# Optimization experiments

Hardware: AMD Instinct MI355X
Metric: run time of the kernel (lower is better)

## Reference

```python
import jax, jax.numpy as jnp
import numpy as np

P = 2          # SamplesLoss p=2
BLUR = 0.05    # eps_final = BLUR**P = 0.0025
SCALING = 0.8  # annealing factor per iteration (on the blur scale)


def _cost(x, y):
    # geomloss cost for p=2: |x - y|^2 / 2, shape (N, M)
    x2 = jnp.sum(x * x, axis=-1)
    y2 = jnp.sum(y * y, axis=-1)
    return 0.5 * (x2[:, None] + y2[None, :] - 2.0 * (x @ y.T))


def _softmin(eps, C, h):
    # -eps * log sum_j exp(h_j - C_ij / eps); h already contains log-weights
    return -eps * jax.nn.logsumexp(h[None, :] - C / eps, axis=1)


def _eps_schedule(x, y):
    # geomloss scaling_parameters / epsilon_schedule with diameter from bounding box
    xn, yn = np.asarray(x), np.asarray(y)
    mins = np.minimum(xn.min(0), yn.min(0))
    maxs = np.maximum(xn.max(0), yn.max(0))
    diameter = float(np.linalg.norm(maxs - mins))
    eps_list = ([diameter ** P]
                + [float(np.exp(e)) for e in np.arange(P * np.log(diameter), P * np.log(BLUR), P * np.log(SCALING))]
                + [BLUR ** P])
    return eps_list


def _sinkhorn_divergence(x, y, eps_list):
    # Debiased Sinkhorn divergence S_eps(x, y), geomloss sinkhorn_tensorized
    N, M = x.shape[0], y.shape[0]
    sg = jax.lax.stop_gradient
    C_xy, C_yx = _cost(x, y), _cost(y, x)
    C_xx, C_yy = _cost(x, sg(x)), _cost(y, sg(y))  # geomloss detaches 2nd arg
    # The annealing loop runs with autograd disabled in geomloss:
    Cxy_, Cyx_, Cxx_, Cyy_ = sg(C_xy), sg(C_yx), sg(C_xx), sg(C_yy)
    a_log = jnp.full((N,), -np.log(N), dtype=x.dtype)  # log uniform weights
    b_log = jnp.full((M,), -np.log(M), dtype=y.dtype)
    e0 = eps_list[0]
    f_aa = _softmin(e0, Cxx_, a_log)
    g_bb = _softmin(e0, Cyy_, b_log)
    g_ab = _softmin(e0, Cyx_, a_log)
    f_ba = _softmin(e0, Cxy_, b_log)
    for eps in eps_list:  # fixed schedule, not a data-dim loop
        ft_ba = _softmin(eps, Cxy_, b_log + g_ab / eps)
        gt_ab = _softmin(eps, Cyx_, a_log + f_ba / eps)
        ft_aa = _softmin(eps, Cxx_, a_log + f_aa / eps)
        gt_bb = _softmin(eps, Cyy_, b_log + g_bb / eps)
        f_ba, g_ab = 0.5 * (f_ba + ft_ba), 0.5 * (g_ab + gt_ab)
        f_aa, g_bb = 0.5 * (f_aa + ft_aa), 0.5 * (g_bb + gt_bb)
    # Final extrapolation step (the only one geomloss differentiates through):
    eps = eps_list[-1]
    f_ba, g_ab = (_softmin(eps, C_xy, sg(b_log + g_ab / eps)),
                  _softmin(eps, C_yx, sg(a_log + f_ba / eps)))
    f_aa = _softmin(eps, C_xx, sg(a_log + f_aa / eps))
    g_bb = _softmin(eps, C_yy, sg(b_log + g_bb / eps))
    # scal with uniform weights == mean
    return jnp.mean(f_ba - f_aa) + jnp.mean(g_ab - g_bb)


def setup_inputs() -> dict:
    key = jax.random.key(0)
    kx, kt = jax.random.split(key)
    x = jax.random.normal(kx, (4096, 64), dtype=jnp.float32)
    target = jax.random.normal(kt, (4096, 64), dtype=jnp.float32)
    return {"x": x, "target": target}


def reference(x, target):
    eps_list = _eps_schedule(x, target)  # concrete schedule from data diameter
    return _sinkhorn_divergence(x, target, eps_list)
```

## Files before the change

### kernel.cpp

```cpp
#include <hip/hip_runtime.h>
#include <math.h>

#define NPTS 4096
#define DIM  64
#define MAX_ITERS 37

#define ALOG (-8.317766166719343f)
#define L2E  (1.4426950408889634f)
#define LN2  (0.6931471805599453f)

#define SEA 8388608.0f
#define SEB 1064872507.0f

#if __has_builtin(__builtin_amdgcn_exp2f)
#define EXP2F(x) __builtin_amdgcn_exp2f(x)
#else
#define EXP2F(x) exp2f(x)
#endif
#if __has_builtin(__builtin_amdgcn_logf)
#define LOG2F(x) __builtin_amdgcn_logf(x)
#else
#define LOG2F(x) log2f(x)
#endif

typedef _Float16 f16x8 __attribute__((ext_vector_type(8)));
typedef float    f32x4 __attribute__((ext_vector_type(4)));

__device__ __forceinline__ float aload(const float* p) {
    return __hip_atomic_load(p, __ATOMIC_RELAXED, __HIP_MEMORY_SCOPE_AGENT);
}
__device__ __forceinline__ void astore(float* p, float v) {
    __hip_atomic_store(p, v, __ATOMIC_RELAXED, __HIP_MEMORY_SCOPE_AGENT);
}

template <bool FENCE>
__device__ __forceinline__ void gbar(int* st, int idx, int nsub, int* lsense) {
    __syncthreads();
    if (threadIdx.x == 0) {
        int s = *lsense ^ 1;
        if (FENCE) __threadfence();
        int sub = idx >> 5;
        int prev = __hip_atomic_fetch_add(st + sub * 16, 1, __ATOMIC_ACQ_REL,
                                          __HIP_MEMORY_SCOPE_AGENT);
        if (prev == 31) {
            int pm = __hip_atomic_fetch_add(st + 1536, 1, __ATOMIC_ACQ_REL,
                                            __HIP_MEMORY_SCOPE_AGENT);
            if (pm == nsub - 1) {
                for (int i = 0; i < nsub; i++)
                    __hip_atomic_store(st + i * 16, 0, __ATOMIC_RELAXED,
                                       __HIP_MEMORY_SCOPE_AGENT);
                __hip_atomic_store(st + 1536, 0, __ATOMIC_RELAXED,
                                   __HIP_MEMORY_SCOPE_AGENT);
                __hip_atomic_store(st + 1600, s, __ATOMIC_RELEASE,
                                   __HIP_MEMORY_SCOPE_AGENT);
            } else {
                while (__hip_atomic_load(st + 1600, __ATOMIC_ACQUIRE,
                                         __HIP_MEMORY_SCOPE_AGENT) != s)
                    __builtin_amdgcn_s_sleep(8);
            }
        } else {
            while (__hip_atomic_load(st + 1600, __ATOMIC_ACQUIRE,
                                     __HIP_MEMORY_SCOPE_AGENT) != s)
                __builtin_amdgcn_s_sleep(8);
        }
        *lsense = s;
        if (FENCE) __threadfence();
    }
    __syncthreads();
}

__global__ __launch_bounds__(256, 8) void mega9_kernel(
        const float* __restrict__ x, const float* __restrict__ y,
        _Float16* __restrict__ X16, _Float16* __restrict__ Y16,
        float* __restrict__ x2, float* __restrict__ y2,
        float* __restrict__ pmn, float* __restrict__ pmx,
        int* hdr, float* __restrict__ sched,
        float* H, float* P,
        int* bar, float* __restrict__ out)
{
    const int b  = blockIdx.x;
    const int tt = threadIdx.x;
    int senseA = 0, senseB = 0, senseG = 0;

    const int grp = b >> 10;
    int* barA = bar + grp * 2048;
    int* barB = bar + 4096 + grp * 2048;
    int* barG = bar + 8192;
    const int idxL = b & 1023;

    __shared__ float hs[256];
    __shared__ _Float16 Bs[2][64][72];

    {
        int g = b * 256 + tt;
        if (g < NPTS * DIM) {
            float xv = x[g], yv = y[g];
            X16[g] = (_Float16)xv;
            Y16[g] = (_Float16)yv;
            float sx = xv * xv, sy = yv * yv;
            for (int o = 32; o > 0; o >>= 1) {
                sx += __shfl_xor(sx, o, 64);
                sy += __shfl_xor(sy, o, 64);
            }
            if ((tt & 63) == 0) { x2[g >> 6] = sx; y2[g >> 6] = sy; }
        }
        if (b < 128) {
            float mn = INFINITY, mx = -INFINITY;
            for (int gg = b * 256 + tt; gg < NPTS * DIM; gg += 128 * 256) {
                float v = x[gg]; mn = fminf(mn, v); mx = fmaxf(mx, v);
                float w = y[gg]; mn = fminf(mn, w); mx = fmaxf(mx, w);
            }
            float* smn = hs;
            float* smx = (float*)&Bs[0][0][0];
            smn[tt] = mn; smx[tt] = mx;
            __syncthreads();
            if (tt < 64) {
                for (int qq = 1; qq < 4; qq++) {
                    mn = fminf(mn, smn[tt + 64 * qq]);
                    mx = fmaxf(mx, smx[tt + 64 * qq]);
                }
                pmn[b * 64 + tt] = mn;
                pmx[b * 64 + tt] = mx;
            }
        }
    }
    gbar<true>(barG, b, 64, &senseG);

    if (b == 0) {
        float* r2 = hs;
        if (tt < 64) {
            float mn = INFINITY, mx = -INFINITY;
            for (int bb = 0; bb < 128; bb++) {
                mn = fminf(mn, pmn[bb * 64 + tt]);
                mx = fmaxf(mx, pmx[bb * 64 + tt]);
            }
            float range = mx - mn;
            r2[tt] = range * range;
        }
        __syncthreads();
        if (tt == 0) {
            float ss = 0.f;
            for (int k = 0; k < 64; k++) ss += r2[k];
            float diam_f = sqrtf(ss);
            double diam = (double)diam_f;
            double start = 2.0 * log(diam);
            double stop  = 2.0 * log(0.05);
            double step  = 2.0 * log(0.8);
            int n_ar = (int)ceil((stop - start) / step);
            if (n_ar < 0) n_ar = 0;
            int ne = n_ar + 2;
            if (ne > 63) ne = 63;
// ... 113 lines not shown
#pragma unroll
        for (int rt = 0; rt < 2; rt++)
            s[rt] *= EXP2F(ml[rt] - m[rt]);
#pragma unroll
        for (int off = 16; off < 64; off <<= 1)
#pragma unroll
            for (int rt = 0; rt < 2; rt++)
                s[rt] += __shfl_xor(s[rt], off, 64);

        if (q == 0) {
            int pw = (t == -1) ? (n_eps & 1) : ((t == -2) ? 1 : (t & 1));
            float* Pw = P + pw * 524288;
            float* Sw = Pw + 262144;
#pragma unroll
            for (int rt = 0; rt < 2; rt++) {
                int row = r0 + wv * 32 + rt * 16 + lo;
                astore(&Pw[(mat * 16 + cs) * NPTS + row], m[rt]);
                astore(&Sw[(mat * 16 + cs) * NPTS + row], s[rt]);
            }
        }
        __syncthreads();
    };

    run_main(-2);
    for (int c = 0; c <= n_eps; c++) {
        gbar<false>(barA, idxL, 32, &senseA);
        if (isComb) {
            int pp = (c == 0) ? 1 : ((c - 1) & 1);
            const float* Pm = P + pp * 524288;
            const float* Ps = Pm + 262144;
            float epsp  = sched[(c == 0) ? 0 : (c - 1)];
            float inv2c = L2E / sched[c];
            int base = (matc * 16) * NPTS + combRow;
            float M = -INFINITY, S = 0.f;
#pragma unroll
            for (int qq = 0; qq < 16; qq++) {
                float pv = aload(&Pm[base + qq * NPTS]);
                float sv = aload(&Ps[base + qq * NPTS]);
                if (pv > M) { S *= EXP2F(M - pv); M = pv; }
                S += sv * EXP2F(pv - M);
            }
            float res  = 0.5f * combSq - epsp * LN2 * (M + LOG2F(S));
            float fnew = (c == 0) ? res : 0.5f * (fprev + res);
            fprev = fnew;
            astore(&H[mat * 4096 + combRow],
                   ALOG * L2E + (fnew - 0.5f * combSq) * inv2c);
        }
        gbar<false>(barB, idxL, 32, &senseB);
        if (c < n_eps) run_main(c);
    }
    run_main(-1);

    gbar<true>(barG, b, 64, &senseG);

    if (b < 64) {
        const float* Pm = P + (n_eps & 1) * 524288;
        const float* Ps = Pm + 262144;
        int g = b * 256 + tt;
        int fmat = g >> 12, row = g & 4095;
        float eps = sched[n_eps - 1];
        const float* sqr = (fmat == 0 || fmat == 2) ? x2 : y2;
        int base = (fmat * 16) * NPTS + row;
        float M = -INFINITY, S = 0.f;
#pragma unroll
        for (int qq = 0; qq < 16; qq++) {
            float pv = aload(&Pm[base + qq * NPTS]);
            float sv = aload(&Ps[base + qq * NPTS]);
            if (pv > M) { S *= EXP2F(M - pv); M = pv; }
            S += sv * EXP2F(pv - M);
        }
        float res = 0.5f * sqr[row] - eps * LN2 * (M + LOG2F(S));
        float val = ((fmat < 2) ? res : -res) * (1.0f / NPTS);
        float* sh = hs;
        sh[tt] = val;
        __syncthreads();
        for (int o = 128; o > 0; o >>= 1) {
            if (tt < o) sh[tt] += sh[tt + o];
            __syncthreads();
        }
        if (tt == 0) atomicAdd(out, sh[0]);
    }
}

__device__ __forceinline__ void multi_barrier(int* st, int idx, int nsub,
                                              int* lsense) {
    __syncthreads();
    if (threadIdx.x == 0) {
        int s = *lsense ^ 1;
        __threadfence();
        int sub = idx >> 5;
        int prev = __hip_atomic_fetch_add(st + sub * 16, 1, __ATOMIC_ACQ_REL,
                                          __HIP_MEMORY_SCOPE_AGENT);
        if (prev == 31) {
            int pm = __hip_atomic_fetch_add(st + 512, 1, __ATOMIC_ACQ_REL,
                                            __HIP_MEMORY_SCOPE_AGENT);
            if (pm == nsub - 1) {
                for (int i = 0; i < nsub; i++)
                    __hip_atomic_store(st + i * 16, 0, __ATOMIC_RELAXED,
                                       __HIP_MEMORY_SCOPE_AGENT);
                __hip_atomic_store(st + 512, 0, __ATOMIC_RELAXED,
                                   __HIP_MEMORY_SCOPE_AGENT);
                __hip_atomic_store(st + 544, s, __ATOMIC_RELEASE,
                                   __HIP_MEMORY_SCOPE_AGENT);
            } else {
                while (__hip_atomic_load(st + 544, __ATOMIC_ACQUIRE,
                                         __HIP_MEMORY_SCOPE_AGENT) != s)
                    __builtin_amdgcn_s_sleep(8);
            }
        } else {
            while (__hip_atomic_load(st + 544, __ATOMIC_ACQUIRE,
                                     __HIP_MEMORY_SCOPE_AGENT) != s)
                __builtin_amdgcn_s_sleep(8);
        }
        *lsense = s;
        __threadfence();
    }
    __syncthreads();
}

template <int TPB>
__global__ __launch_bounds__(256, (TPB == 1 ? 4 : 2)) void mega_kernel(
        const float* __restrict__ x, const float* __restrict__ y,
        _Float16* __restrict__ X16, _Float16* __restrict__ Y16,
        float* __restrict__ x2, float* __restrict__ y2,
        float* __restrict__ pmn, float* __restrict__ pmx,
        int* hdr, float* __restrict__ sched,
        float* __restrict__ F, float* __restrict__ H, float* __restrict__ P,
        int* bar, float* __restrict__ out)
{
    const int b  = blockIdx.x;
    const int tt = threadIdx.x;
    int senseG = 0, senseL = 0;

    int* stG;  int nsubG;
    int* stL;  int idxL; int nsubL;
    if (TPB == 1) {
        stG = bar + 2048; nsubG = 32;
        stL = bar + (b >> 9) * 1024; idxL = b & 511; nsubL = 16;
    } else {
        stG = bar + 2048; nsubG = 16;
        stL = stG; idxL = b; nsubL = 16;
    }
    int* senseLp = (TPB == 1) ? &senseL : &senseG;

    __shared__ float hs[512];
    __shared__ _Float16 Bs[2][64][72];

    for (int g = b * 256 + tt; g < NPTS * DIM; g += gridDim.x * 256) {
        float xv = x[g], yv = y[g];
        X16[g] = (_Float16)xv;
        Y16[g] = (_Float16)yv;
        float sx = xv * xv, sy = yv * yv;
        for (int o = 32; o > 0; o >>= 1) {
            sx += __shfl_xor(sx, o, 64);
            sy += __shfl_xor(sy, o, 64);
        }
        if ((tt & 63) == 0) { x2[g >> 6] = sx; y2[g >> 6] = sy; }
    }
    if (b < 128) {
        float mn = INFINITY, mx = -INFINITY;
        for (int gg = b * 256 + tt; gg < NPTS * DIM; gg += 128 * 256) {
            float v = x[gg]; mn = fminf(mn, v); mx = fmaxf(mx, v);
            float w = y[gg]; mn = fminf(mn, w); mx = fmaxf(mx, w);
        }
        float* smn = hs;
        float* smx = (float*)&Bs[0][0][0];
        smn[tt] = mn; smx[tt] = mx;
        __syncthreads();
        if (tt < 64) {
            for (int qq = 1; qq < 4; qq++) {
                mn = fminf(mn, smn[tt + 64 * qq]);
                mx = fmaxf(mx, smx[tt + 64 * qq]);
            }
            pmn[b * 64 + tt] = mn;
            pmx[b * 64 + tt] = mx;
        }
    }
    multi_barrier(stG, b, nsubG, &senseG);

    if (b == 0) {
        float* r2 = hs;
        if (tt < 64) {
            float mn = INFINITY, mx = -INFINITY;
            for (int bb = 0; bb < 128; bb++) {
                mn = fminf(mn, pmn[bb * 64 + tt]);
                mx = fmaxf(mx, pmx[bb * 64 + tt]);
            }
            float range = mx - mn;
            r2[tt] = range * range;
        }
        __syncthreads();
        if (tt == 0) {
            float ss = 0.f;
            for (int k = 0; k < 64; k++) ss += r2[k];
            float diam_f = sqrtf(ss);
            double diam = (double)diam_f;
            double start = 2.0 * log(diam);
            double stop  = 2.0 * log(0.05);
            double step  = 2.0 * log(0.8);
            int n_ar = (int)ceil((stop - start) / step);
            if (n_ar < 0) n_ar = 0;
            int ne = n_ar + 2;
            if (ne > 63) ne = 63;
            sched[0] = (float)(diam * diam);
            for (int k = 0; k < n_ar && (1 + k) < 63; k++)
                sched[1 + k] = (float)exp(start + step * (double)k);
            sched[ne - 1] = 0.0025f;
            for (int k = ne; k < 64; k++) sched[k] = 0.0025f;
            hdr[0] = ne;
        }
    }
    multi_barrier(stG, b, nsubG, &senseG);

    const int n_eps = *(volatile int*)hdr;

    const int wv = tt >> 6, lane = tt & 63, q = lane >> 4, lo = lane & 15;
    const int srow = tt >> 2, scol = (tt & 3) * 16;

    f16x8 a[TPB][2][2];
#pragma unroll
    for (int sub = 0; sub < TPB; sub++) {
        const int bt = b + 512 * sub;
        const int mat_ = bt >> 8, rb_ = (bt >> 3) & 31;
        const _Float16* Am = (mat_ == 0 || mat_ == 2) ? X16 : Y16;
        const int r0_ = rb_ * 128;
#pragma unroll
        for (int rt = 0; rt < 2; rt++) {
            const _Float16* ar = Am + (size_t)(r0_ + wv * 32 + rt * 16 + lo) * DIM + q * 8;
            a[sub][rt][0] = *(const f16x8*)ar;
            a[sub][rt][1] = *(const f16x8*)(ar + 32);
        }
    }

    for (int p = 0; p <= n_eps + 2; p++) {
        const int t = (p == 0) ? -2 : (p == n_eps + 2) ? -1 : (p - 1);
        const bool do_main = (t < 0) || (t < n_eps);

#pragma unroll
        for (int sub = 0; sub < TPB; sub++) {
            const int bt = b + 512 * sub;
            const int mat = bt >> 8, rb = (bt >> 3) & 31, cs = bt & 7;
            const _Float16* Bm = (mat == 1 || mat == 2) ? X16 : Y16;
            const int matc = (mat < 2) ? (1 - mat) : mat;
            const float* sqc = (matc == 0 || matc == 2) ? x2 : y2;
            const int c0 = cs * 512, r0 = rb * 128;
            const _Float16* Bsrc0 = Bm + (size_t)(c0 + srow) * DIM + scol;

            f16x8 t0a, t0b;
            if (do_main) {
                t0a = *(const f16x8*)Bsrc0;
                t0b = *(const f16x8*)(Bsrc0 + 8);
            }

            if (t == -2) {
                float inv2i = L2E / sched[0];
                for (int r = tt; r < 512; r += 256)
                    hs[r] = ALOG * L2E - 0.5f * sqc[c0 + r] * inv2i;
            } else if (t == -1) {
                for (int r = tt; r < 512; r += 256)
                    hs[r] = H[mat * 4096 + c0 + r];
            } else {
                int pp = (t == 0) ? 1 : ((t - 1) & 1);
                const float* Pm = P + pp * 262144;
                const float* Ps = Pm + 131072;
                float epsp = sched[(t == 0) ? 0 : (t - 1)];
                float inv2c = L2E / sched[t];
                for (int r = tt; r < 512; r += 256) {
                    int row = c0 + r;
                    int base = (matc * 8) * NPTS + row;
                    float M = -INFINITY;
#pragma unroll
                    for (int qq = 0; qq < 8; qq++) M = fmaxf(M, Pm[base + qq * NPTS]);
                    float S = 0.f;
#pragma unroll
                    for (int qq = 0; qq < 8; qq++)
                        S += Ps[base + qq * NPTS] * EXP2F(Pm[base + qq * NPTS] - M);
                    float sq = sqc[row];
                    float res = 0.5f * sq - epsp * LN2 * (M + LOG2F(S));
                    float fnew = (t == 0) ? res
                               : 0.5f * (F[((t - 1) & 1) * 16384 + matc * 4096 + row] + res);
                    float h = ALOG * L2E + (fnew - 0.5f * sq) * inv2c;
                    hs[r] = h;
                    if (rb == 0) {
                        F[(t & 1) * 16384 + matc * 4096 + row] = fnew;
                        H[mat * 4096 + row] = h;
                    }
                }
            }

            if (do_main) {
                int idx = (t == -2) ? 0 : ((t == -1) ? n_eps - 1 : t);
                float inv2 = L2E / sched[idx];

                *(f16x8*)&Bs[0][srow][scol]     = t0a;
                *(f16x8*)&Bs[0][srow][scol + 8] = t0b;

                float m[2][4], s[2][4];
#pragma unroll
                for (int rt = 0; rt < 2; rt++)
#pragma unroll
                    for (int r = 0; r < 4; r++) { m[rt][r] = -INFINITY; s[rt][r] = 0.f; }

                for (int ct = 0; ct < 8; ct++) {
                    __syncthreads();
                    f16x8 n0, n1;
                    if (ct < 7) {
                        const _Float16* src = Bsrc0 + (size_t)(ct + 1) * 64 * DIM;
                        n0 = *(const f16x8*)src;
                        n1 = *(const f16x8*)(src + 8);
                    }
                    const _Float16 (*Bt)[72] = Bs[ct & 1];
                    float v[2][4][4];
#pragma unroll
                    for (int cc = 0; cc < 4; cc++) {
                        const _Float16* br = &Bt[cc * 16 + lo][q * 8];
                        f16x8 b0 = *(const f16x8*)br;
                        f16x8 b1 = *(const f16x8*)(br + 32);
                        float hval = hs[ct * 64 + cc * 16 + lo];
#pragma unroll
                        for (int rt = 0; rt < 2; rt++) {
                            f32x4 acc = {0.f, 0.f, 0.f, 0.f};
                            acc = __builtin_amdgcn_mfma_f32_16x16x32_f16(a[sub][rt][0], b0, acc, 0, 0, 0);
                            acc = __builtin_amdgcn_mfma_f32_16x16x32_f16(a[sub][rt][1], b1, acc, 0, 0, 0);
#pragma unroll
                            for (int r = 0; r < 4; r++) v[rt][r][cc] = fmaf(acc[r], inv2, hval);
                        }
                    }
#pragma unroll
                    for (int rt = 0; rt < 2; rt++)
#pragma unroll
                        for (int r = 0; r < 4; r++) {
                            float v0 = v[rt][r][0], v1 = v[rt][r][1];
                            float v2 = v[rt][r][2], v3 = v[rt][r][3];
                            float lm = fmaxf(fmaxf(v0, v1), fmaxf(v2, v3));
                            if (__any(lm > m[rt][r] + 40.0f)) {
                                float nm = fmaxf(m[rt][r], lm);
                                s[rt][r] *= EXP2F(m[rt][r] - nm);
                                m[rt][r] = nm;
                            }
                            if (lm > m[rt][r] - 26.0f) {
                                float mm = m[rt][r];
                                s[rt][r] += (EXP2F(v0 - mm) + EXP2F(v1 - mm))
                                          + (EXP2F(v2 - mm) + EXP2F(v3 - mm));
                            }
                        }
                    if (ct < 7) {
                        *(f16x8*)&Bs[(ct + 1) & 1][srow][scol]     = n0;
                        *(f16x8*)&Bs[(ct + 1) & 1][srow][scol + 8] = n1;
                    }
                }

                float ml[2][4];
#pragma unroll
                for (int rt = 0; rt < 2; rt++)
#pragma unroll
                    for (int r = 0; r < 4; r++) ml[rt][r] = m[rt][r];
#pragma unroll
                for (int off = 1; off < 16; off <<= 1)
#pragma unroll
                    for (int rt = 0; rt < 2; rt++)
#pragma unroll
                        for (int r = 0; r < 4; r++)
                            m[rt][r] = fmaxf(m[rt][r], __shfl_xor(m[rt][r], off, 64));
#pragma unroll
                for (int rt = 0; rt < 2; rt++)
#pragma unroll
                    for (int r = 0; r < 4; r++)
                        s[rt][r] *= EXP2F(ml[rt][r] - m[rt][r]);
#pragma unroll
                for (int off = 1; off < 16; off <<= 1)
#pragma unroll
                    for (int rt = 0; rt < 2; rt++)
#pragma unroll
                        for (int r = 0; r < 4; r++)
                            s[rt][r] += __shfl_xor(s[rt][r], off, 64);

                if (lo == 0) {
                    int pw = (t == -1) ? (n_eps & 1) : ((t == -2) ? 1 : (t & 1));
                    float* Pw = P + pw * 262144;
                    float* Sw = Pw + 131072;
#pragma unroll
                    for (int rt = 0; rt < 2; rt++)
#pragma unroll
                        for (int r = 0; r < 4; r++) {
                            int row = r0 + wv * 32 + rt * 16 + q * 4 + r;
                            Pw[(mat * 8 + cs) * NPTS + row] = m[rt][r];
                            Sw[(mat * 8 + cs) * NPTS + row] = s[rt][r];
                        }
                }
            }
            __syncthreads();
        }
        multi_barrier(stL, idxL, nsubL, senseLp);
    }

    multi_barrier(stG, b, nsubG, &senseG);

    if (b < 64) {
        const float* Pm = P + (n_eps & 1) * 262144;
        const float* Ps = Pm + 131072;
        int g = b * 256 + tt;
        int fmat = g >> 12, row = g & 4095;
        float eps = sched[n_eps - 1];
        const float* sqr = (fmat == 0 || fmat == 2) ? x2 : y2;
        int base = (fmat * 8) * NPTS + row;
        float M = -INFINITY;
#pragma unroll
        for (int qq = 0; qq < 8; qq++) M = fmaxf(M, Pm[base + qq * NPTS]);
        float S = 0.f;
#pragma unroll
        for (int qq = 0; qq < 8; qq++)
            S += Ps[base + qq * NPTS] * EXP2F(Pm[base + qq * NPTS] - M);
        float res = 0.5f * sqr[row] - eps * LN2 * (M + LOG2F(S));
        float val = ((fmat < 2) ? res : -res) * (1.0f / NPTS);
        float* sh = hs;
        sh[tt] = val;
        __syncthreads();
        for (int o = 128; o > 0; o >>= 1) {
            if (tt < o) sh[tt] += sh[tt + o];
            __syncthreads();
        }
        if (tt == 0) atomicAdd(out, sh[0]);
    }
}

__global__ void minmax_part_kernel(const float* __restrict__ x,
                                   const float* __restrict__ y,
                                   float* __restrict__ partmn,
                                   float* __restrict__ partmx) {
    int t = threadIdx.x;
    int bid = blockIdx.x;
    int g0 = bid * 256 + t;
    const int total = NPTS * DIM;
    float mn = INFINITY, mx = -INFINITY;
    for (int g = g0; g < total; g += 128 * 256) {
        float v = x[g]; mn = fminf(mn, v); mx = fmaxf(mx, v);
        float w = y[g]; mn = fminf(mn, w); mx = fmaxf(mx, w);
    }
    __shared__ float smn[256], smx[256];
    smn[t] = mn; smx[t] = mx;
    __syncthreads();
    if (t < 64) {
        for (int q = 1; q < 4; q++) {
            mn = fminf(mn, smn[t + 64 * q]);
            mx = fmaxf(mx, smx[t + 64 * q]);
        }
        partmn[bid * 64 + t] = mn;
        partmx[bid * 64 + t] = mx;
    }
}

__global__ void schedule_kernel(const float* __restrict__ partmn,
                                const float* __restrict__ partmx,
                                int* __restrict__ hdr,
                                float* __restrict__ sched) {
    int d = threadIdx.x;
    float mn = INFINITY, mx = -INFINITY;
    for (int b = 0; b < 128; b++) {
        mn = fminf(mn, partmn[b * 64 + d]);
        mx = fmaxf(mx, partmx[b * 64 + d]);
    }
    float range = mx - mn;
    __shared__ float r2[64];
    r2[d] = range * range;
    __syncthreads();
    if (d == 0) {
        float ss = 0.f;
        for (int k = 0; k < 64; k++) ss += r2[k];
        float diam_f = sqrtf(ss);
        double diam = (double)diam_f;
        double start = 2.0 * log(diam);
        double stop  = 2.0 * log(0.05);
        double step  = 2.0 * log(0.8);
        int n_eps = (int)ceil((stop - start) / step);
        if (n_eps < 0) n_eps = 0;
        n_eps += 2;
        if (n_eps > 63) n_eps = 63;
        sched[0] = (float)(diam * diam);
        for (int k = 0; k < n_eps - 2 && (1 + k) < 63; k++)
            sched[1 + k] = (float)exp(start + step * (double)k);
        sched[n_eps - 1] = 0.0025f;
        for (int k = n_eps; k < 64; k++) sched[k] = 0.0025f;
        hdr[0] = n_eps;
    }
}

__global__ void sqnorm_kernel(const float* __restrict__ X, float* __restrict__ out) {
    int wave = (blockIdx.x * blockDim.x + threadIdx.x) >> 6;
    int lane = threadIdx.x & 63;
    if (wave >= NPTS) return;
    float v = X[wave * DIM + lane];
    float s = v * v;
    for (int o = 32; o > 0; o >>= 1) s += __shfl_xor(s, o, 64);
    if (lane == 0) out[wave] = s;
}

__global__ void cast_kernel(const float* __restrict__ x, const float* __restrict__ y,
                            _Float16* __restrict__ X16, _Float16* __restrict__ Y16) {
    int g = blockIdx.x * 256 + threadIdx.x;
    X16[g] = (_Float16)x[g];
    Y16[g] = (_Float16)y[g];
}

__global__ __launch_bounds__(256, 4) void pass_kernel(
        const _Float16* __restrict__ X16, const _Float16* __restrict__ Y16,
        const float* __restrict__ x2, const float* __restrict__ y2,
        float* __restrict__ F, float* __restrict__ H, float* __restrict__ P,
        const int* __restrict__ hdr, const float* __restrict__ sched, int t) {
// ... 120 lines not shown
            *(f16x8*)&Bs[(ct + 1) & 1][srow][scol]     = n0;
            *(f16x8*)&Bs[(ct + 1) & 1][srow][scol + 8] = n1;
        }
    }

#pragma unroll
    for (int off = 1; off < 16; off <<= 1) {
#pragma unroll
        for (int rt = 0; rt < 2; rt++)
#pragma unroll
            for (int r = 0; r < 4; r++) {
                float om = __shfl_xor(m[rt][r], off, 64);
                float os = __shfl_xor(s[rt][r], off, 64);
                float nm = fmaxf(m[rt][r], om);
                s[rt][r] = s[rt][r] * EXP2F(m[rt][r] - nm) + os * EXP2F(om - nm);
                m[rt][r] = nm;
            }
    }
    if (lo == 0) {
        int pw = (t == -1) ? (n_eps & 1) : ((t == -2) ? 1 : (t & 1));
        float* Pm = P + pw * 262144;
        float* Ps = Pm + 131072;
#pragma unroll
        for (int rt = 0; rt < 2; rt++)
#pragma unroll
            for (int r = 0; r < 4; r++) {
                int row = r0 + wv * 32 + rt * 16 + q * 4 + r;
                Pm[(mat * 8 + cs) * NPTS + row] = m[rt][r];
                Ps[(mat * 8 + cs) * NPTS + row] = s[rt][r];
            }
    }
}

__global__ void finalize_kernel(const float* __restrict__ P,
                                const float* __restrict__ x2, const float* __restrict__ y2,
                                const int* __restrict__ hdr, const float* __restrict__ sched,
                                float* __restrict__ out) {
    int n_eps = hdr[0];
    const float* Pm = P + (n_eps & 1) * 262144;
    const float* Ps = Pm + 131072;
    int g = blockIdx.x * 256 + threadIdx.x;
    int mat = g >> 12, row = g & 4095;
    float eps = sched[n_eps - 1];
    const float* sqr = (mat == 0 || mat == 2) ? x2 : y2;
    int base = (mat * 8) * NPTS + row;
    float M = -INFINITY;
#pragma unroll
    for (int q = 0; q < 8; q++) M = fmaxf(M, Pm[base + q * NPTS]);
    float S = 0.f;
#pragma unroll
    for (int q = 0; q < 8; q++) S += Ps[base + q * NPTS] * EXP2F(Pm[base + q * NPTS] - M);
    float res = 0.5f * sqr[row] - eps * LN2 * (M + LOG2F(S));
    float val = ((mat == 0 || mat == 1) ? res : -res) * (1.0f / NPTS);
    __shared__ float sh[256];
    sh[threadIdx.x] = val;
    __syncthreads();
    for (int o = 128; o > 0; o >>= 1) {
        if (threadIdx.x < o) sh[threadIdx.x] += sh[threadIdx.x + o];
        __syncthreads();
    }
    if (threadIdx.x == 0) atomicAdd(out, sh[0]);
}

extern "C" void kernel_launch(void* const* d_in, const int* in_sizes, int n_in,
                              void* d_out, int out_size, void* d_ws, size_t ws_size,
                              hipStream_t stream) {
    const float* x = (const float*)d_in[0];
    const float* y = (const float*)d_in[1];
    float* out = (float*)d_out;
    float* w = (float*)d_ws;

    int*   hdr   = (int*)w;
    float* sched = w + 16;
    float* pmn   = w + 80;
    float* pmx   = w + 8272;
    float* x2    = w + 16464;
    float* y2    = w + 20560;
    float* F     = w + 24656;
    float* H     = w + 57424;
    float* P     = w + 73808;

    _Float16* X16c = (_Float16*)(w + 598096);
    _Float16* Y16c = (_Float16*)(w + 729168);
    int*      barc = (int*)(w + 860240);

    _Float16* X16e = (_Float16*)(w + 1122384);
    _Float16* Y16e = (_Float16*)(w + 1253456);
    int*      bare = (int*)(w + 1384528);
    const size_t ws_need_e = (size_t)(1384528 + 10240 + 16) * 4;

    hipMemsetAsync(out, 0, sizeof(float), stream);

    int occ9 = 0, occ1 = 0, occ2 = 0;
    (void)hipOccupancyMaxActiveBlocksPerMultiprocessor(&occ9, mega9_kernel, 256, 0);
    (void)hipOccupancyMaxActiveBlocksPerMultiprocessor(&occ1, mega_kernel<1>, 256, 0);
    (void)hipOccupancyMaxActiveBlocksPerMultiprocessor(&occ2, mega_kernel<2>, 256, 0);

    if (occ9 >= 8 && ws_size >= ws_need_e) {
        hipMemsetAsync(bare, 0, 5 * 2048 * sizeof(int), stream);
        hipLaunchKernelGGL(mega9_kernel, dim3(2048), dim3(256), 0, stream,
                           x, y, X16e, Y16e, x2, y2, pmn, pmx, hdr, sched,
                           H, P, bare, out);
    } else if (occ1 >= 4) {
        hipMemsetAsync(barc, 0, 3 * 1024 * sizeof(int), stream);
        hipLaunchKernelGGL((mega_kernel<1>), dim3(1024), dim3(256), 0, stream,
                           x, y, X16c, Y16c, x2, y2, pmn, pmx, hdr, sched,
                           F, H, P, barc, out);
    } else if (occ2 >= 2) {
        hipMemsetAsync(barc, 0, 3 * 1024 * sizeof(int), stream);
        hipLaunchKernelGGL((mega_kernel<2>), dim3(512), dim3(256), 0, stream,
                           x, y, X16c, Y16c, x2, y2, pmn, pmx, hdr, sched,
                           F, H, P, barc, out);
    } else {
        hipLaunchKernelGGL(minmax_part_kernel, dim3(128), dim3(256), 0, stream, x, y, pmn, pmx);
        hipLaunchKernelGGL(schedule_kernel, dim3(1), dim3(64), 0, stream, pmn, pmx, hdr, sched);
        hipLaunchKernelGGL(sqnorm_kernel, dim3(1024), dim3(256), 0, stream, x, x2);
        hipLaunchKernelGGL(sqnorm_kernel, dim3(1024), dim3(256), 0, stream, y, y2);
        hipLaunchKernelGGL(cast_kernel, dim3(1024), dim3(256), 0, stream, x, y, X16c, Y16c);
        hipLaunchKernelGGL(pass_kernel, dim3(1024), dim3(256), 0, stream,
                           X16c, Y16c, x2, y2, F, H, P, hdr, sched, -2);
        for (int t = 0; t < MAX_ITERS; t++)
            hipLaunchKernelGGL(pass_kernel, dim3(1024), dim3(256), 0, stream,
                               X16c, Y16c, x2, y2, F, H, P, hdr, sched, t);
        hipLaunchKernelGGL(pass_kernel, dim3(1024), dim3(256), 0, stream,
                           X16c, Y16c, x2, y2, F, H, P, hdr, sched, -1);
        hipLaunchKernelGGL(finalize_kernel, dim3(64), dim3(256), 0, stream,
                           P, x2, y2, hdr, sched, out);
    }
}
```

Baseline: 956.3 us.

## Add 1024-block persistent kernel with 256x256 tiles and bit-trick exp

Adds a new persistent kernel that uses 1024 blocks at occupancy 4, each handling a 256-row by 256-column tile, in place of the 2048-block mega9 design with smaller tiles. This halves the number of blocks taking part in each grid barrier and raises per-block data reuse. Inside the logsumexp loop, exp2 is approximated with a float-bit-construction trick rather than the hardware exp. Barrier spin sleep is shortened from 8 to 2, and the older mega_kernel fallback paths are removed. Costs include more register pressure from a larger A fragment, longer per-block work between barriers, and lower accuracy from the approximate exp.

```diff
diff --git a/kernel.cpp b/kernel.cpp
--- a/kernel.cpp
+++ b/kernel.cpp
@@ -56,17 +56,302 @@
             } else {
                 while (__hip_atomic_load(st + 1600, __ATOMIC_ACQUIRE,
                                          __HIP_MEMORY_SCOPE_AGENT) != s)
-                    __builtin_amdgcn_s_sleep(8);
+                    __builtin_amdgcn_s_sleep(2);
             }
         } else {
             while (__hip_atomic_load(st + 1600, __ATOMIC_ACQUIRE,
                                      __HIP_MEMORY_SCOPE_AGENT) != s)
-                __builtin_amdgcn_s_sleep(8);
+                __builtin_amdgcn_s_sleep(2);
         }
         *lsense = s;
         if (FENCE) __threadfence();
     }
     __syncthreads();
+}
+
+__global__ __launch_bounds__(256, 4) void mega10_kernel(
+        const float* __restrict__ x, const float* __restrict__ y,
+        _Float16* __restrict__ X16, _Float16* __restrict__ Y16,
+        float* __restrict__ x2, float* __restrict__ y2,
+        float* __restrict__ pmn, float* __restrict__ pmx,
+        int* hdr, float* __restrict__ sched,
+        float* H, float* P,
+        int* bar, float* __restrict__ out)
+{
+    const int b  = blockIdx.x;
+    const int tt = threadIdx.x;
+    int senseA = 0, senseB = 0, senseG = 0;
+
+    const int grp = b >> 9;
+    int* barA = bar + grp * 2048;
+    int* barB = bar + 4096 + grp * 2048;
+    int* barG = bar + 8192;
+    const int idxL = b & 511;
+
+    __shared__ float hs[256];
+    __shared__ _Float16 Bs[2][64][72];
+
+    {
+        int g = b * 256 + tt;
+        if (g < NPTS * DIM) {
+            float xv = x[g], yv = y[g];
+            X16[g] = (_Float16)xv;
+            Y16[g] = (_Float16)yv;
+            float sx = xv * xv, sy = yv * yv;
+            for (int o = 32; o > 0; o >>= 1) {
+                sx += __shfl_xor(sx, o, 64);
+                sy += __shfl_xor(sy, o, 64);
+            }
+            if ((tt & 63) == 0) { x2[g >> 6] = sx; y2[g >> 6] = sy; }
+        }
+        if (b < 128) {
+            float mn = INFINITY, mx = -INFINITY;
+            for (int gg = b * 256 + tt; gg < NPTS * DIM; gg += 128 * 256) {
+                float v = x[gg]; mn = fminf(mn, v); mx = fmaxf(mx, v);
+                float w = y[gg]; mn = fminf(mn, w); mx = fmaxf(mx, w);
+            }
+            float* smn = hs;
+            float* smx = (float*)&Bs[0][0][0];
+            smn[tt] = mn; smx[tt] = mx;
+            __syncthreads();
+            if (tt < 64) {
+                for (int qq = 1; qq < 4; qq++) {
+                    mn = fminf(mn, smn[tt + 64 * qq]);
+                    mx = fmaxf(mx, smx[tt + 64 * qq]);
+                }
+                pmn[b * 64 + tt] = mn;
+                pmx[b * 64 + tt] = mx;
+            }
+        }
+    }
+    gbar<true>(barG, b, 32, &senseG);
+
+    if (b == 0) {
+        float* r2 = hs;
+        if (tt < 64) {
+            float mn = INFINITY, mx = -INFINITY;
+            for (int bb = 0; bb < 128; bb++) {
+                mn = fminf(mn, pmn[bb * 64 + tt]);
+                mx = fmaxf(mx, pmx[bb * 64 + tt]);
+            }
+            float range = mx - mn;
+            r2[tt] = range * range;
+        }
+        __syncthreads();
+        if (tt == 0) {
+            float ss = 0.f;
+            for (int k = 0; k < 64; k++) ss += r2[k];
+            float diam_f = sqrtf(ss);
+            double diam = (double)diam_f;
+            double start = 2.0 * log(diam);
+            double stop  = 2.0 * log(0.05);
+            double step  = 2.0 * log(0.8);
+            int n_ar = (int)ceil((stop - start) / step);
+            if (n_ar < 0) n_ar = 0;
+            int ne = n_ar + 2;
+            if (ne > 63) ne = 63;
+            sched[0] = (float)(diam * diam);
+            for (int k = 0; k < n_ar && (1 + k) < 63; k++)
+                sched[1 + k] = (float)exp(start + step * (double)k);
+            sched[ne - 1] = 0.0025f;
+            for (int k = ne; k < 64; k++) sched[k] = 0.0025f;
+            hdr[0] = ne;
+        }
+    }
+    gbar<true>(barG, b, 32, &senseG);
+
+    const int n_eps = *(volatile int*)hdr;
+
+    const int mat = b >> 8, rb = (b >> 4) & 15, cs = b & 15;
+    const _Float16* Am = (mat == 0 || mat == 2) ? X16 : Y16;
+    const _Float16* Bm = (mat == 1 || mat == 2) ? X16 : Y16;
+    const int matc = (mat < 2) ? (1 - mat) : mat;
+    const float* sqc = (matc == 0 || matc == 2) ? x2 : y2;
+    const int c0 = cs * 256, r0 = rb * 256;
+    const int wv = tt >> 6, lane = tt & 63, q = lane >> 4, lo = lane & 15;
+    const int srow = tt >> 2, scol = (tt & 3) * 16;
+
+    f16x8 a[4][2];
+#pragma unroll
+    for (int rt = 0; rt < 4; rt++) {
+        const _Float16* ar = Am + (size_t)(r0 + wv * 64 + rt * 16 + lo) * DIM + q * 8;
+        a[rt][0] = *(const f16x8*)ar;
+        a[rt][1] = *(const f16x8*)(ar + 32);
+    }
+    const _Float16* Bsrc0 = Bm + (size_t)(c0 + srow) * DIM + scol;
+
+    const bool isComb = (rb < 4) && (tt < 64);
+    int   combRow = 0;
+    float combSq = 0.f, fprev = 0.f;
+    if (rb < 4) {
+        combRow = (cs * 4 + rb) * 64 + (tt & 63);
+        combSq  = sqc[combRow];
+    }
+
+    auto run_main = [&](int t) {
+        f16x8 t0a = *(const f16x8*)Bsrc0;
+        f16x8 t0b = *(const f16x8*)(Bsrc0 + 8);
+
+        if (t == -2) {
+            float inv2i = L2E / sched[0];
+            hs[tt] = ALOG * L2E - 0.5f * sqc[c0 + tt] * inv2i;
+        } else {
+            hs[tt] = aload(&H[mat * 4096 + c0 + tt]);
+        }
+
+        int idx = (t == -2) ? 0 : ((t == -1) ? n_eps - 1 : t);
+        float inv2 = L2E / sched[idx];
+
+        *(f16x8*)&Bs[0][srow][scol]     = t0a;
+        *(f16x8*)&Bs[0][srow][scol + 8] = t0b;
+
+        float m[4] = { -1e30f, -1e30f, -1e30f, -1e30f };
+        float s[4] = { 0.f, 0.f, 0.f, 0.f };
+
+        for (int ct = 0; ct < 4; ct++) {
+            __syncthreads();
+            f16x8 n0, n1;
+            if (ct < 3) {
+                const _Float16* src = Bsrc0 + (size_t)(ct + 1) * 64 * DIM;
+                n0 = *(const f16x8*)src;
+                n1 = *(const f16x8*)(src + 8);
+            }
+            const _Float16 (*Bt)[72] = Bs[ct & 1];
+#pragma unroll
+            for (int cc = 0; cc < 4; cc++) {
+                const _Float16* br = &Bt[cc * 16 + lo][q * 8];
+                f16x8 b0 = *(const f16x8*)br;
+                f16x8 b1 = *(const f16x8*)(br + 32);
+                f32x4 hv = *(const f32x4*)&hs[ct * 64 + cc * 16 + q * 4];
+#pragma unroll
+                for (int rt = 0; rt < 4; rt++) {
+                    f32x4 acc = {0.f, 0.f, 0.f, 0.f};
+                    acc = __builtin_amdgcn_mfma_f32_16x16x32_f16(b0, a[rt][0], acc, 0, 0, 0);
+                    acc = __builtin_amdgcn_mfma_f32_16x16x32_f16(b1, a[rt][1], acc, 0, 0, 0);
+                    float v0 = fmaf(acc[0], inv2, hv[0]);
+                    float v1 = fmaf(acc[1], inv2, hv[1]);
+                    float v2 = fmaf(acc[2], inv2, hv[2]);
+                    float v3 = fmaf(acc[3], inv2, hv[3]);
+                    float lm = fmaxf(fmaxf(v0, v1), fmaxf(v2, v3));
+                    if (__any(lm > m[rt] + 40.0f)) {
+                        float nm = fmaxf(m[rt], lm);
+                        s[rt] *= EXP2F(m[rt] - nm);
+                        m[rt] = nm;
+                    }
+                    if (lm > m[rt] - 126.0f) {
+                        float mm = m[rt];
+                        float e0 = fmaxf(fmaf(v0 - mm, SEA, SEB), 0.f);
+                        float e1 = fmaxf(fmaf(v1 - mm, SEA, SEB), 0.f);
+                        float e2 = fmaxf(fmaf(v2 - mm, SEA, SEB), 0.f);
+                        float e3 = fmaxf(fmaf(v3 - mm, SEA, SEB), 0.f);
+                        s[rt] += (__uint_as_float((unsigned)e0)
+                                + __uint_as_float((unsigned)e1))
+                               + (__uint_as_float((unsigned)e2)
+                                + __uint_as_float((unsigned)e3));
+                    }
+                }
+            }
+            if (ct < 3) {
+                *(f16x8*)&Bs[(ct + 1) & 1][srow][scol]     = n0;
+                *(f16x8*)&Bs[(ct + 1) & 1][srow][scol + 8] = n1;
+            }
+        }
+
+        float ml[4] = { m[0], m[1], m[2], m[3] };
+#pragma unroll
+        for (int off = 16; off < 64; off <<= 1)
+#pragma unroll
+            for (int rt = 0; rt < 4; rt++)
+                m[rt] = fmaxf(m[rt], __shfl_xor(m[rt], off, 64));
+#pragma unroll
+        for (int rt = 0; rt < 4; rt++)
+            s[rt] *= EXP2F(ml[rt] - m[rt]);
+#pragma unroll
+        for (int off = 16; off < 64; off <<= 1)
+#pragma unroll
+            for (int rt = 0; rt < 4; rt++)
+                s[rt] += __shfl_xor(s[rt], off, 64);
+
+        if (q == 0) {
+            int pw = (t == -1) ? (n_eps & 1) : ((t == -2) ? 1 : (t & 1));
+            float* Pw = P + pw * 524288;
+            float* Sw = Pw + 262144;
+#pragma unroll
+            for (int rt = 0; rt < 4; rt++) {
+                int row = r0 + wv * 64 + rt * 16 + lo;
+                astore(&Pw[(mat * 16 + cs) * NPTS + row], m[rt]);
+                astore(&Sw[(mat * 16 + cs) * NPTS + row], s[rt]);
+            }
+        }
+        __syncthreads();
+    };
+
+    run_main(-2);
+    for (int c = 0; c <= n_eps; c++) {
+        gbar<false>(barA, idxL, 16, &senseA);
+        if (isComb) {
+            int pp = (c == 0) ? 1 : ((c - 1) & 1);
+            const float* Pm = P + pp * 524288;
+            const float* Ps = Pm + 262144;
+            float epsp  = sched[(c == 0) ? 0 : (c - 1)];
+            float inv2c = L2E / sched[c];
+            int base = (matc * 16) * NPTS + combRow;
+            float pv[16], sv[16];
+#pragma unroll
+            for (int qq = 0; qq < 16; qq++) {
+                pv[qq] = aload(&Pm[base + qq * NPTS]);
+                sv[qq] = aload(&Ps[base + qq * NPTS]);
+            }
+            float M = -INFINITY, S = 0.f;
+#pragma unroll
+            for (int qq = 0; qq < 16; qq++) {
+                if (pv[qq] > M) { S *= EXP2F(M - pv[qq]); M = pv[qq]; }
+                S += sv[qq] * EXP2F(pv[qq] - M);
+            }
+            float res  = 0.5f * combSq - epsp * LN2 * (M + LOG2F(S));
+            float fnew = (c == 0) ? res : 0.5f * (fprev + res);
+            fprev = fnew;
+            astore(&H[mat * 4096 + combRow],
+                   ALOG * L2E + (fnew - 0.5f * combSq) * inv2c);
+        }
+        gbar<false>(barB, idxL, 16, &senseB);
+        if (c < n_eps) run_main(c);
+    }
+    run_main(-1);
+
+    gbar<true>(barG, b, 32, &senseG);
+
+    if (b < 64) {
+        const float* Pm = P + (n_eps & 1) * 524288;
+        const float* Ps = Pm + 262144;
+        int g = b * 256 + tt;
+        int fmat = g >> 12, row = g & 4095;
+        float eps = sched[n_eps - 1];
+        const float* sqr = (fmat == 0 || fmat == 2) ? x2 : y2;
+        int base = (fmat * 16) * NPTS + row;
+        float pv[16], sv[16];
+#pragma unroll
+        for (int qq = 0; qq < 16; qq++) {
+            pv[qq] = aload(&Pm[base + qq * NPTS]);
+            sv[qq] = aload(&Ps[base + qq * NPTS]);
+        }
+        float M = -INFINITY, S = 0.f;
+#pragma unroll
+        for (int qq = 0; qq < 16; qq++) {
+            if (pv[qq] > M) { S *= EXP2F(M - pv[qq]); M = pv[qq]; }
+            S += sv[qq] * EXP2F(pv[qq] - M);
+        }
+        float res = 0.5f * sqr[row] - eps * LN2 * (M + LOG2F(S));
+        float val = ((fmat < 2) ? res : -res) * (1.0f / NPTS);
+        float* sh = hs;
+        sh[tt] = val;
+        __syncthreads();
+        for (int o = 128; o > 0; o >>= 1) {
+            if (tt < o) sh[tt] += sh[tt + o];
+            __syncthreads();
+        }
+        if (tt == 0) atomicAdd(out, sh[0]);
+    }
 }
 
 __global__ __launch_bounds__(256, 8) void mega9_kernel(
@@ -346,348 +631,6 @@
     }
 }
 
-__device__ __forceinline__ void multi_barrier(int* st, int idx, int nsub,
-                                              int* lsense) {
-    __syncthreads();
-    if (threadIdx.x == 0) {
-        int s = *lsense ^ 1;
-        __threadfence();
-        int sub = idx >> 5;
-        int prev = __hip_atomic_fetch_add(st + sub * 16, 1, __ATOMIC_ACQ_REL,
-                                          __HIP_MEMORY_SCOPE_AGENT);
-        if (prev == 31) {
-            int pm = __hip_atomic_fetch_add(st + 512, 1, __ATOMIC_ACQ_REL,
-                                            __HIP_MEMORY_SCOPE_AGENT);
-            if (pm == nsub - 1) {
-                for (int i = 0; i < nsub; i++)
-                    __hip_atomic_store(st + i * 16, 0, __ATOMIC_RELAXED,
-                                       __HIP_MEMORY_SCOPE_AGENT);
-                __hip_atomic_store(st + 512, 0, __ATOMIC_RELAXED,
-                                   __HIP_MEMORY_SCOPE_AGENT);
-                __hip_atomic_store(st + 544, s, __ATOMIC_RELEASE,
-                                   __HIP_MEMORY_SCOPE_AGENT);
-            } else {
-                while (__hip_atomic_load(st + 544, __ATOMIC_ACQUIRE,
-                                         __HIP_MEMORY_SCOPE_AGENT) != s)
-                    __builtin_amdgcn_s_sleep(8);
-            }
-        } else {
-            while (__hip_atomic_load(st + 544, __ATOMIC_ACQUIRE,
-                                     __HIP_MEMORY_SCOPE_AGENT) != s)
-                __builtin_amdgcn_s_sleep(8);
-        }
-        *lsense = s;
-        __threadfence();
-    }
-    __syncthreads();
-}
-
-template <int TPB>
-__global__ __launch_bounds__(256, (TPB == 1 ? 4 : 2)) void mega_kernel(
-        const float* __restrict__ x, const float* __restrict__ y,
-        _Float16* __restrict__ X16, _Float16* __restrict__ Y16,
-        float* __restrict__ x2, float* __restrict__ y2,
-        float* __restrict__ pmn, float* __restrict__ pmx,
-        int* hdr, float* __restrict__ sched,
-        float* __restrict__ F, float* __restrict__ H, float* __restrict__ P,
-        int* bar, float* __restrict__ out)
-{
-    const int b  = blockIdx.x;
-    const int tt = threadIdx.x;
-    int senseG = 0, senseL = 0;
-
-    int* stG;  int nsubG;
-    int* stL;  int idxL; int nsubL;
-    if (TPB == 1) {
-        stG = bar + 2048; nsubG = 32;
-        stL = bar + (b >> 9) * 1024; idxL = b & 511; nsubL = 16;
-    } else {
-        stG = bar + 2048; nsubG = 16;
-        stL = stG; idxL = b; nsubL = 16;
-    }
-    int* senseLp = (TPB == 1) ? &senseL : &senseG;
-
-    __shared__ float hs[512];
-    __shared__ _Float16 Bs[2][64][72];
-
-    for (int g = b * 256 + tt; g < NPTS * DIM; g += gridDim.x * 256) {
-        float xv = x[g], yv = y[g];
-        X16[g] = (_Float16)xv;
-        Y16[g] = (_Float16)yv;
-        float sx = xv * xv, sy = yv * yv;
-        for (int o = 32; o > 0; o >>= 1) {
-            sx += __shfl_xor(sx, o, 64);
-            sy += __shfl_xor(sy, o, 64);
-        }
-        if ((tt & 63) == 0) { x2[g >> 6] = sx; y2[g >> 6] = sy; }
-    }
-    if (b < 128) {
-        float mn = INFINITY, mx = -INFINITY;
-        for (int gg = b * 256 + tt; gg < NPTS * DIM; gg += 128 * 256) {
-            float v = x[gg]; mn = fminf(mn, v); mx = fmaxf(mx, v);
-            float w = y[gg]; mn = fminf(mn, w); mx = fmaxf(mx, w);
-        }
-        float* smn = hs;
-        float* smx = (float*)&Bs[0][0][0];
-        smn[tt] = mn; smx[tt] = mx;
-        __syncthreads();
-        if (tt < 64) {
-            for (int qq = 1; qq < 4; qq++) {
-                mn = fminf(mn, smn[tt + 64 * qq]);
-                mx = fmaxf(mx, smx[tt + 64 * qq]);
-            }
-            pmn[b * 64 + tt] = mn;
-            pmx[b * 64 + tt] = mx;
-        }
-    }
-    multi_barrier(stG, b, nsubG, &senseG);
-
-    if (b == 0) {
-        float* r2 = hs;
-        if (tt < 64) {
-            float mn = INFINITY, mx = -INFINITY;
-            for (int bb = 0; bb < 128; bb++) {
-                mn = fminf(mn, pmn[bb * 64 + tt]);
-                mx = fmaxf(mx, pmx[bb * 64 + tt]);
-            }
-            float range = mx - mn;
-            r2[tt] = range * range;
-        }
-        __syncthreads();
-        if (tt == 0) {
-            float ss = 0.f;
-            for (int k = 0; k < 64; k++) ss += r2[k];
-            float diam_f = sqrtf(ss);
-            double diam = (double)diam_f;
-            double start = 2.0 * log(diam);
-            double stop  = 2.0 * log(0.05);
-            double step  = 2.0 * log(0.8);
-            int n_ar = (int)ceil((stop - start) / step);
-            if (n_ar < 0) n_ar = 0;
-            int ne = n_ar + 2;
-            if (ne > 63) ne = 63;
-            sched[0] = (float)(diam * diam);
-            for (int k = 0; k < n_ar && (1 + k) < 63; k++)
-                sched[1 + k] = (float)exp(start + step * (double)k);
-            sched[ne - 1] = 0.0025f;
-            for (int k = ne; k < 64; k++) sched[k] = 0.0025f;
-            hdr[0] = ne;
-        }
-    }
-    multi_barrier(stG, b, nsubG, &senseG);
-
-    const int n_eps = *(volatile int*)hdr;
-
-    const int wv = tt >> 6, lane = tt & 63, q = lane >> 4, lo = lane & 15;
-    const int srow = tt >> 2, scol = (tt & 3) * 16;
-
-    f16x8 a[TPB][2][2];
-#pragma unroll
-    for (int sub = 0; sub < TPB; sub++) {
-        const int bt = b + 512 * sub;
-        const int mat_ = bt >> 8, rb_ = (bt >> 3) & 31;
-        const _Float16* Am = (mat_ == 0 || mat_ == 2) ? X16 : Y16;
-        const int r0_ = rb_ * 128;
-#pragma unroll
-        for (int rt = 0; rt < 2; rt++) {
-            const _Float16* ar = Am + (size_t)(r0_ + wv * 32 + rt * 16 + lo) * DIM + q * 8;
-            a[sub][rt][0] = *(const f16x8*)ar;
-            a[sub][rt][1] = *(const f16x8*)(ar + 32);
-        }
-    }
-
-    for (int p = 0; p <= n_eps + 2; p++) {
-        const int t = (p == 0) ? -2 : (p == n_eps + 2) ? -1 : (p - 1);
-        const bool do_main = (t < 0) || (t < n_eps);
-
-#pragma unroll
-        for (int sub = 0; sub < TPB; sub++) {
-            const int bt = b + 512 * sub;
-            const int mat = bt >> 8, rb = (bt >> 3) & 31, cs = bt & 7;
-            const _Float16* Bm = (mat == 1 || mat == 2) ? X16 : Y16;
-            const int matc = (mat < 2) ? (1 - mat) : mat;
-            const float* sqc = (matc == 0 || matc == 2) ? x2 : y2;
-            const int c0 = cs * 512, r0 = rb * 128;
-            const _Float16* Bsrc0 = Bm + (size_t)(c0 + srow) * DIM + scol;
-
-            f16x8 t0a, t0b;
-            if (do_main) {
-                t0a = *(const f16x8*)Bsrc0;
-                t0b = *(const f16x8*)(Bsrc0 + 8);
-            }
-
-            if (t == -2) {
-                float inv2i = L2E / sched[0];
-                for (int r = tt; r < 512; r += 256)
-                    hs[r] = ALOG * L2E - 0.5f * sqc[c0 + r] * inv2i;
-            } else if (t == -1) {
-                for (int r = tt; r < 512; r += 256)
-                    hs[r] = H[mat * 4096 + c0 + r];
-            } else {
-                int pp = (t == 0) ? 1 : ((t - 1) & 1);
-                const float* Pm = P + pp * 262144;
-                const float* Ps = Pm + 131072;
-                float epsp = sched[(t == 0) ? 0 : (t - 1)];
-                float inv2c = L2E / sched[t];
-                for (int r = tt; r < 512; r += 256) {
-                    int row = c0 + r;
-                    int base = (matc * 8) * NPTS + row;
-                    float M = -INFINITY;
-#pragma unroll
-                    for (int qq = 0; qq < 8; qq++) M = fmaxf(M, Pm[base + qq * NPTS]);
-                    float S = 0.f;
-#pragma unroll
-                    for (int qq = 0; qq < 8; qq++)
-                        S += Ps[base + qq * NPTS] * EXP2F(Pm[base + qq * NPTS] - M);
-                    float sq = sqc[row];
-                    float res = 0.5f * sq - epsp * LN2 * (M + LOG2F(S));
-                    float fnew = (t == 0) ? res
-                               : 0.5f * (F[((t - 1) & 1) * 16384 + matc * 4096 + row] + res);
-                    float h = ALOG * L2E + (fnew - 0.5f * sq) * inv2c;
-                    hs[r] = h;
-                    if (rb == 0) {
-                        F[(t & 1) * 16384 + matc * 4096 + row] = fnew;
-                        H[mat * 4096 + row] = h;
-                    }
-                }
-            }
-
-            if (do_main) {
-                int idx = (t == -2) ? 0 : ((t == -1) ? n_eps - 1 : t);
-                float inv2 = L2E / sched[idx];
-
-                *(f16x8*)&Bs[0][srow][scol]     = t0a;
-                *(f16x8*)&Bs[0][srow][scol + 8] = t0b;
-
-                float m[2][4], s[2][4];
-#pragma unroll
-                for (int rt = 0; rt < 2; rt++)
-#pragma unroll
-                    for (int r = 0; r < 4; r++) { m[rt][r] = -INFINITY; s[rt][r] = 0.f; }
-
-                for (int ct = 0; ct < 8; ct++) {
-                    __syncthreads();
-                    f16x8 n0, n1;
-                    if (ct < 7) {
-                        const _Float16* src = Bsrc0 + (size_t)(ct + 1) * 64 * DIM;
-                        n0 = *(const f16x8*)src;
-                        n1 = *(const f16x8*)(src + 8);
-                    }
-                    const _Float16 (*Bt)[72] = Bs[ct & 1];
-                    float v[2][4][4];
-#pragma unroll
-                    for (int cc = 0; cc < 4; cc++) {
-                        const _Float16* br = &Bt[cc * 16 + lo][q * 8];
-                        f16x8 b0 = *(const f16x8*)br;
-                        f16x8 b1 = *(const f16x8*)(br + 32);
-                        float hval = hs[ct * 64 + cc * 16 + lo];
-#pragma unroll
-                        for (int rt = 0; rt < 2; rt++) {
-                            f32x4 acc = {0.f, 0.f, 0.f, 0.f};
-                            acc = __builtin_amdgcn_mfma_f32_16x16x32_f16(a[sub][rt][0], b0, acc, 0, 0, 0);
-                            acc = __builtin_amdgcn_mfma_f32_16x16x32_f16(a[sub][rt][1], b1, acc, 0, 0, 0);
-#pragma unroll
-                            for (int r = 0; r < 4; r++) v[rt][r][cc] = fmaf(acc[r], inv2, hval);
-                        }
-                    }
-#pragma unroll
-                    for (int rt = 0; rt < 2; rt++)
-#pragma unroll
-                        for (int r = 0; r < 4; r++) {
-                            float v0 = v[rt][r][0], v1 = v[rt][r][1];
-                            float v2 = v[rt][r][2], v3 = v[rt][r][3];
-                            float lm = fmaxf(fmaxf(v0, v1), fmaxf(v2, v3));
-                            if (__any(lm > m[rt][r] + 40.0f)) {
-                                float nm = fmaxf(m[rt][r], lm);
-                                s[rt][r] *= EXP2F(m[rt][r] - nm);
-                                m[rt][r] = nm;
-                            }
-                            if (lm > m[rt][r] - 26.0f) {
-                                float mm = m[rt][r];
-                                s[rt][r] += (EXP2F(v0 - mm) + EXP2F(v1 - mm))
-                                          + (EXP2F(v2 - mm) + EXP2F(v3 - mm));
-                            }
-                        }
-                    if (ct < 7) {
-                        *(f16x8*)&Bs[(ct + 1) & 1][srow][scol]     = n0;
-                        *(f16x8*)&Bs[(ct + 1) & 1][srow][scol + 8] = n1;
-                    }
-                }
-
-                float ml[2][4];
-#pragma unroll
-                for (int rt = 0; rt < 2; rt++)
-#pragma unroll
-                    for (int r = 0; r < 4; r++) ml[rt][r] = m[rt][r];
-#pragma unroll
-                for (int off = 1; off < 16; off <<= 1)
-#pragma unroll
-                    for (int rt = 0; rt < 2; rt++)
-#pragma unroll
-                        for (int r = 0; r < 4; r++)
-                            m[rt][r] = fmaxf(m[rt][r], __shfl_xor(m[rt][r], off, 64));
-#pragma unroll
-                for (int rt = 0; rt < 2; rt++)
-#pragma unroll
-                    for (int r = 0; r < 4; r++)
-                        s[rt][r] *= EXP2F(ml[rt][r] - m[rt][r]);
-#pragma unroll
-                for (int off = 1; off < 16; off <<= 1)
-#pragma unroll
-                    for (int rt = 0; rt < 2; rt++)
-#pragma unroll
-                        for (int r = 0; r < 4; r++)
-                            s[rt][r] += __shfl_xor(s[rt][r], off, 64);
-
-                if (lo == 0) {
-                    int pw = (t == -1) ? (n_eps & 1) : ((t == -2) ? 1 : (t & 1));
-                    float* Pw = P + pw * 262144;
-                    float* Sw = Pw + 131072;
-#pragma unroll
-                    for (int rt = 0; rt < 2; rt++)
-#pragma unroll
-                        for (int r = 0; r < 4; r++) {
-                            int row = r0 + wv * 32 + rt * 16 + q * 4 + r;
-                            Pw[(mat * 8 + cs) * NPTS + row] = m[rt][r];
-                            Sw[(mat * 8 + cs) * NPTS + row] = s[rt][r];
-                        }
-                }
-            }
-            __syncthreads();
-        }
-        multi_barrier(stL, idxL, nsubL, senseLp);
-    }
-
-    multi_barrier(stG, b, nsubG, &senseG);
-
-    if (b < 64) {
-        const float* Pm = P + (n_eps & 1) * 262144;
-        const float* Ps = Pm + 131072;
-        int g = b * 256 + tt;
-        int fmat = g >> 12, row = g & 4095;
-        float eps = sched[n_eps - 1];
-        const float* sqr = (fmat == 0 || fmat == 2) ? x2 : y2;
-        int base = (fmat * 8) * NPTS + row;
-        float M = -INFINITY;
-#pragma unroll
-        for (int qq = 0; qq < 8; qq++) M = fmaxf(M, Pm[base + qq * NPTS]);
-        float S = 0.f;
-#pragma unroll
-        for (int qq = 0; qq < 8; qq++)
-            S += Ps[base + qq * NPTS] * EXP2F(Pm[base + qq * NPTS] - M);
-        float res = 0.5f * sqr[row] - eps * LN2 * (M + LOG2F(S));
-        float val = ((fmat < 2) ? res : -res) * (1.0f / NPTS);
-        float* sh = hs;
-        sh[tt] = val;
-        __syncthreads();
-        for (int o = 128; o > 0; o >>= 1) {
-            if (tt < o) sh[tt] += sh[tt + o];
-            __syncthreads();
-        }
-        if (tt == 0) atomicAdd(out, sh[0]);
-    }
-}
-
 __global__ void minmax_part_kernel(const float* __restrict__ x,
                                    const float* __restrict__ y,
                                    float* __restrict__ partmn,
@@ -974,7 +917,6 @@
 
     _Float16* X16c = (_Float16*)(w + 598096);
     _Float16* Y16c = (_Float16*)(w + 729168);
-    int*      barc = (int*)(w + 860240);
 
     _Float16* X16e = (_Float16*)(w + 1122384);
     _Float16* Y16e = (_Float16*)(w + 1253456);
@@ -983,26 +925,20 @@
 
     hipMemsetAsync(out, 0, sizeof(float), stream);
 
-    int occ9 = 0, occ1 = 0, occ2 = 0;
+    int occ10 = 0, occ9 = 0;
+    (void)hipOccupancyMaxActiveBlocksPerMultiprocessor(&occ10, mega10_kernel, 256, 0);
     (void)hipOccupancyMaxActiveBlocksPerMultiprocessor(&occ9, mega9_kernel, 256, 0);
-    (void)hipOccupancyMaxActiveBlocksPerMultiprocessor(&occ1, mega_kernel<1>, 256, 0);
-    (void)hipOccupancyMaxActiveBlocksPerMultiprocessor(&occ2, mega_kernel<2>, 256, 0);
-
-    if (occ9 >= 8 && ws_size >= ws_need_e) {
+
+    if (occ10 >= 4 && ws_size >= ws_need_e) {
+        hipMemsetAsync(bare, 0, 5 * 2048 * sizeof(int), stream);
+        hipLaunchKernelGGL(mega10_kernel, dim3(1024), dim3(256), 0, stream,
+                           x, y, X16e, Y16e, x2, y2, pmn, pmx, hdr, sched,
+                           H, P, bare, out);
+    } else if (occ9 >= 8 && ws_size >= ws_need_e) {
         hipMemsetAsync(bare, 0, 5 * 2048 * sizeof(int), stream);
         hipLaunchKernelGGL(mega9_kernel, dim3(2048), dim3(256), 0, stream,
                            x, y, X16e, Y16e, x2, y2, pmn, pmx, hdr, sched,
                            H, P, bare, out);
-    } else if (occ1 >= 4) {
-        hipMemsetAsync(barc, 0, 3 * 1024 * sizeof(int), stream);
-        hipLaunchKernelGGL((mega_kernel<1>), dim3(1024), dim3(256), 0, stream,
-                           x, y, X16c, Y16c, x2, y2, pmn, pmx, hdr, sched,
-                           F, H, P, barc, out);
-    } else if (occ2 >= 2) {
-        hipMemsetAsync(barc, 0, 3 * 1024 * sizeof(int), stream);
-        hipLaunchKernelGGL((mega_kernel<2>), dim3(512), dim3(256), 0, stream,
-                           x, y, X16c, Y16c, x2, y2, pmn, pmx, hdr, sched,
-                           F, H, P, barc, out);
     } else {
         hipLaunchKernelGGL(minmax_part_kernel, dim3(128), dim3(256), 0, stream, x, y, pmn, pmx);
         hipLaunchKernelGGL(schedule_kernel, dim3(1), dim3(64), 0, stream, pmn, pmx, hdr, sched);
```

Measured after the change: 956.9 us. About the same (+0.1%).
